# Kernel optimization log

Hardware: AMD Instinct MI355X
Metric: run time of the kernel (lower is better)

Reference implementation:

```python
import jax, jax.numpy as jnp
import numpy as np

TEMPERATURE = 0.1
EPS = 1e-8  # torch CosineSimilarity eps


def setup_inputs() -> dict:
    key = jax.random.key(0)
    y = jax.random.normal(key, (8192, 256), dtype=jnp.float32)
    return {"y": y}


def reference(y):
    # y: (2n, d), rows 2i and 2i+1 are positive pairs
    N = y.shape[0]
    norms = jnp.maximum(jnp.linalg.norm(y, axis=1, keepdims=True), EPS)
    yn = y / norms  # (N, d)
    sim = yn @ yn.T  # (N, N) cosine similarity
    e = jnp.exp(sim / TEMPERATURE)
    # denominator: column-sum excluding diagonal (mask eye==0)
    denom = e.sum(axis=0) - jnp.diagonal(e)  # (N,)
    # positive pair index: row 2i -> 2i+1, row 2i+1 -> 2i (XOR with 1)
    row_idx = jnp.arange(N)
    col_idx = row_idx ^ 1
    pos = e[row_idx, col_idx]  # (N,)
    loss = -jnp.log(pos / denom)
    return loss.mean()
```

## Files before the change

### kernel.cpp

```cpp
#include <hip/hip_runtime.h>
#include <hip/hip_bf16.h>
#include <cstdint>

typedef __attribute__((ext_vector_type(4))) float f32x4;

#define DIM 256
#define TINV 10.0f
#define EXP2C 14.426950408889634f
#define BM 128
#define BN 128
#define BK 64
#define NSLOT 64
#define NRED 128

__global__ void nt_normalize(const float* __restrict__ y, uint8_t* __restrict__ ynq,
                             int N) {
    int tid = threadIdx.x;
    int wave = tid >> 6, lane = tid & 63;
    int row = blockIdx.x * 4 + wave;
    float4 v = ((const float4*)(y + (size_t)row * DIM))[lane];
    float ss = v.x * v.x + v.y * v.y + v.z * v.z + v.w * v.w;
#pragma unroll
    for (int off = 1; off < 64; off <<= 1) ss += __shfl_xor(ss, off);
    float inv = 1.0f / fmaxf(sqrtf(ss), 1e-8f);
    int w = __builtin_amdgcn_cvt_pk_fp8_f32(v.x * inv, v.y * inv, 0, false);
    w = __builtin_amdgcn_cvt_pk_fp8_f32(v.z * inv, v.w * inv, w, true);
    ((int*)(ynq + (size_t)row * DIM))[lane] = w;
}

__launch_bounds__(512, 8)
__global__ void nt_gemm(const uint8_t* __restrict__ ynq, float* __restrict__ P,
                        float* __restrict__ posterm, int N) {
    const int nt = N / BN;
    const int T = nt * (nt + 1) / 2;
    int orig = blockIdx.x;
    int q = T >> 3, r = T & 7;
    int xcd = orig & 7, loc = orig >> 3;
    int t = (xcd < r ? xcd * (q + 1) : r * (q + 1) + (xcd - r) * q) + loc;
    int s = T - 1 - t;
    float f = sqrtf(8.0f * (float)s + 1.0f);
    int j = (int)((f - 1.0f) * 0.5f);
    while ((j + 1) * (j + 2) / 2 <= s) ++j;
    while (j * (j + 1) / 2 > s) --j;
    int k = s - j * (j + 1) / 2;
    int by = nt - 1 - j, bx = nt - 1 - k;

    __shared__ __align__(16) uint8_t As[BM * BK];
    __shared__ __align__(16) uint8_t Bs[BN * BK];
    __shared__ float rowpart[4][BM];
    __shared__ float colpart[2][BN];

    int r0 = by * BM, c0 = bx * BN;
    int tid = threadIdx.x;
    int wave = tid >> 6, lane = tid & 63;
    int wr = wave >> 2, wc = wave & 3;
    int l16 = lane & 15, lg = lane >> 4;

    int srow = tid >> 2, scc = tid & 3;
    int sgc = scc ^ ((srow >> 1) & 3);

    int swz[2];
#pragma unroll
    for (int kk = 0; kk < 2; ++kk)
        swz[kk] = (((kk * 2 + (lg >> 1)) ^ ((l16 >> 1) & 3)) * 16) + (lg & 1) * 8;

    int arow[4], brow[2];
#pragma unroll
    for (int m = 0; m < 4; ++m) arow[m] = (wr * 64 + m * 16 + l16) * BK;
#pragma unroll
    for (int n = 0; n < 2; ++n) brow[n] = (wc * 32 + n * 16 + l16) * BK;

    f32x4 acc[4][2] = {};

    for (int k0 = 0; k0 < DIM; k0 += BK) {
        if (k0) __syncthreads();
        {
            const uint8_t* srcA = ynq + (size_t)(r0 + srow) * DIM + k0 + sgc * 16;
            __builtin_amdgcn_global_load_lds(
                (const __attribute__((address_space(1))) uint32_t*)srcA,
                (__attribute__((address_space(3))) uint32_t*)(As + wave * 1024), 16, 0, 0);
            const uint8_t* srcB = ynq + (size_t)(c0 + srow) * DIM + k0 + sgc * 16;
            __builtin_amdgcn_global_load_lds(
                (const __attribute__((address_space(1))) uint32_t*)srcB,
                (__attribute__((address_space(3))) uint32_t*)(Bs + wave * 1024), 16, 0, 0);
        }
        __syncthreads();

#pragma unroll
        for (int kk = 0; kk < 2; ++kk) {
            long a[4], b[2];
#pragma unroll
            for (int m = 0; m < 4; ++m) a[m] = *(const long*)(As + arow[m] + swz[kk]);
#pragma unroll
            for (int n = 0; n < 2; ++n) b[n] = *(const long*)(Bs + brow[n] + swz[kk]);
#pragma unroll
            for (int m = 0; m < 4; ++m)
#pragma unroll
                for (int n = 0; n < 2; ++n)
                    acc[m][n] = __builtin_amdgcn_mfma_f32_16x16x32_fp8_fp8(
                        a[m], b[n], acc[m][n], 0, 0, 0);
        }
    }

    bool diag = (by == bx);
    float colacc0 = 0.0f, colacc1 = 0.0f;
    float rp[16];
#pragma unroll
    for (int m = 0; m < 4; ++m) {
#pragma unroll
        for (int r2 = 0; r2 < 4; ++r2) {
            int grow = r0 + wr * 64 + m * 16 + lg * 4 + r2;
            float s0, s1;
            {
                float S = acc[m][0][r2];
                float e = __builtin_amdgcn_exp2f(S * EXP2C);
                if (diag) {
                    int gcol = c0 + wc * 32 + l16;
                    if (gcol == grow) e = 0.0f;
                    if (gcol == (grow ^ 1)) posterm[grow] = -S * TINV;
                }
                s0 = e; colacc0 += e;
            }
            {
                float S = acc[m][1][r2];
                float e = __builtin_amdgcn_exp2f(S * EXP2C);
                if (diag) {
                    int gcol = c0 + wc * 32 + 16 + l16;
                    if (gcol == grow) e = 0.0f;
                    if (gcol == (grow ^ 1)) posterm[grow] = -S * TINV;
                }
                s1 = e; colacc1 += e;
            }
            rp[m * 4 + r2] = s0 + s1;
        }
    }
    int b0 = l16 & 1, b1 = (l16 >> 1) & 1, b2 = (l16 >> 2) & 1, b3 = (l16 >> 3) & 1;
    float t8[8];
#pragma unroll
    for (int i = 0; i < 8; ++i) {
        float send = b0 ? rp[2 * i] : rp[2 * i + 1];
        float keep = b0 ? rp[2 * i + 1] : rp[2 * i];
        t8[i] = keep + __shfl_xor(send, 1);
    }
    float t4[4];
#pragma unroll
    for (int i = 0; i < 4; ++i) {
        float send = b1 ? t8[2 * i] : t8[2 * i + 1];
        float keep = b1 ? t8[2 * i + 1] : t8[2 * i];
        t4[i] = keep + __shfl_xor(send, 2);
    }
    float t2[2];
#pragma unroll
    for (int i = 0; i < 2; ++i) {
        float send = b2 ? t4[2 * i] : t4[2 * i + 1];
        float keep = b2 ? t4[2 * i + 1] : t4[2 * i];
        t2[i] = keep + __shfl_xor(send, 4);
    }
    {
        float send = b3 ? t2[0] : t2[1];
        float keep = b3 ? t2[1] : t2[0];
        float rsum = keep + __shfl_xor(send, 8);
        int row_w = ((l16 >> 2) & 3) * 16 + lg * 4 + (l16 & 3);
        rowpart[wc][wr * 64 + row_w] = rsum;
    }
    colacc0 += __shfl_xor(colacc0, 16); colacc0 += __shfl_xor(colacc0, 32);
    colacc1 += __shfl_xor(colacc1, 16); colacc1 += __shfl_xor(colacc1, 32);
    if (!diag && lane < 16) {
        colpart[wr][wc * 32 + lane] = colacc0;
        colpart[wr][wc * 32 + 16 + lane] = colacc1;
    }
    __syncthreads();
    if (tid < BM) {
        P[(size_t)bx * N + r0 + tid] =
            rowpart[0][tid] + rowpart[1][tid] + rowpart[2][tid] + rowpart[3][tid];
    } else if (tid < 2 * BM && !diag) {
        int lcol = tid - BM;
        P[(size_t)by * N + c0 + lcol] = colpart[0][lcol] + colpart[1][lcol];
    }
}

__global__ void nt_reduce_final(const float* __restrict__ P,
                                const float* __restrict__ posterm,
                                float* __restrict__ blockpart,
                                unsigned* __restrict__ cnt,
                                float* __restrict__ out, int N) {
    int lane = threadIdx.x;
    int row = blockIdx.x * 64 + lane;
    float s = 0.0f;
#pragma unroll
    for (int jj = 0; jj < NSLOT; ++jj) s += P[(size_t)jj * N + row];
    float v = posterm[row] + logf(s);
#pragma unroll
    for (int off = 1; off < 64; off <<= 1) v += __shfl_xor(v, off);
    unsigned ticket = 0;
    if (lane == 0) {
        blockpart[blockIdx.x] = v;
        __threadfence();
        ticket = atomicAdd(cnt, 1u);
    }
    ticket = __shfl(ticket, 0);
    if ((ticket & (NRED - 1u)) == NRED - 1u) {
        __threadfence();
        float w = __hip_atomic_load(&blockpart[lane], __ATOMIC_RELAXED,
                                    __HIP_MEMORY_SCOPE_AGENT) +
                  __hip_atomic_load(&blockpart[lane + 64], __ATOMIC_RELAXED,
                                    __HIP_MEMORY_SCOPE_AGENT);
#pragma unroll
        for (int off = 1; off < 64; off <<= 1) w += __shfl_xor(w, off);
        if (lane == 0) out[0] = w / (float)N;
    }
}

extern "C" void kernel_launch(void* const* d_in, const int* in_sizes, int n_in,
                              void* d_out, int out_size, void* d_ws, size_t ws_size,
                              hipStream_t stream) {
    const float* y = (const float*)d_in[0];
    int N = in_sizes[0] / DIM;
    int nt = N / BN;
    uint8_t* ynq = (uint8_t*)d_ws;
    float* posterm = (float*)((char*)d_ws + (size_t)N * DIM);
    float* P = posterm + N;
    float* blockpart = P + (size_t)nt * N;
    unsigned* cnt = (unsigned*)(blockpart + NRED);
    float* out = (float*)d_out;

    nt_normalize<<<N / 4, 256, 0, stream>>>(y, ynq, N);
    int T = nt * (nt + 1) / 2;
    nt_gemm<<<T, 512, 0, stream>>>(ynq, P, posterm, N);
    nt_reduce_final<<<NRED, 64, 0, stream>>>(P, posterm, blockpart, cnt, out, N);
}
```

Baseline: 36.38 us.

## Double-buffer LDS tiles with manual vmcnt waits and MFMA priority boost

Splits the A/B shared-memory tiles into two buffers and unrolls the four K steps by hand. The global-to-LDS load for the next K chunk is issued while the current chunk is being multiplied, with explicit vmcnt waits and raw barriers in place of __syncthreads. s_setprio raises wave priority around the MFMA section. The aim is to hide global load latency behind MFMA work. The cost is twice the LDS per block, which may reduce occupancy, and the hand-written waitcnt ordering relies on the compiler not adding or reordering other memory ops.

```diff
diff --git a/kernel.cpp b/kernel.cpp
--- a/kernel.cpp
+++ b/kernel.cpp
@@ -45,8 +45,8 @@
     int k = s - j * (j + 1) / 2;
     int by = nt - 1 - j, bx = nt - 1 - k;
 
-    __shared__ __align__(16) uint8_t As[BM * BK];
-    __shared__ __align__(16) uint8_t Bs[BN * BK];
+    __shared__ __align__(16) uint8_t As[2][BM * BK];
+    __shared__ __align__(16) uint8_t Bs[2][BN * BK];
     __shared__ float rowpart[4][BM];
     __shared__ float colpart[2][BN];
 
@@ -72,35 +72,64 @@
 
     f32x4 acc[4][2] = {};
 
-    for (int k0 = 0; k0 < DIM; k0 += BK) {
-        if (k0) __syncthreads();
-        {
-            const uint8_t* srcA = ynq + (size_t)(r0 + srow) * DIM + k0 + sgc * 16;
-            __builtin_amdgcn_global_load_lds(
-                (const __attribute__((address_space(1))) uint32_t*)srcA,
-                (__attribute__((address_space(3))) uint32_t*)(As + wave * 1024), 16, 0, 0);
-            const uint8_t* srcB = ynq + (size_t)(c0 + srow) * DIM + k0 + sgc * 16;
-            __builtin_amdgcn_global_load_lds(
-                (const __attribute__((address_space(1))) uint32_t*)srcB,
-                (__attribute__((address_space(3))) uint32_t*)(Bs + wave * 1024), 16, 0, 0);
-        }
-        __syncthreads();
-
-#pragma unroll
-        for (int kk = 0; kk < 2; ++kk) {
-            long a[4], b[2];
-#pragma unroll
-            for (int m = 0; m < 4; ++m) a[m] = *(const long*)(As + arow[m] + swz[kk]);
-#pragma unroll
-            for (int n = 0; n < 2; ++n) b[n] = *(const long*)(Bs + brow[n] + swz[kk]);
-#pragma unroll
-            for (int m = 0; m < 4; ++m)
-#pragma unroll
-                for (int n = 0; n < 2; ++n)
-                    acc[m][n] = __builtin_amdgcn_mfma_f32_16x16x32_fp8_fp8(
-                        a[m], b[n], acc[m][n], 0, 0, 0);
-        }
-    }
+#define STAGE(b, k0)                                                                \
+    {                                                                               \
+        const uint8_t* srcA = ynq + (size_t)(r0 + srow) * DIM + (k0) + sgc * 16;    \
+        __builtin_amdgcn_global_load_lds(                                           \
+            (const __attribute__((address_space(1))) uint32_t*)srcA,                \
+            (__attribute__((address_space(3))) uint32_t*)(As[b] + wave * 1024),     \
+            16, 0, 0);                                                              \
+        const uint8_t* srcB = ynq + (size_t)(c0 + srow) * DIM + (k0) + sgc * 16;    \
+        __builtin_amdgcn_global_load_lds(                                           \
+            (const __attribute__((address_space(1))) uint32_t*)srcB,                \
+            (__attribute__((address_space(3))) uint32_t*)(Bs[b] + wave * 1024),     \
+            16, 0, 0);                                                              \
+    }
+
+#define COMPUTE(b)                                                                  \
+    {                                                                               \
+        __builtin_amdgcn_s_setprio(1);                                              \
+        _Pragma("unroll")                                                           \
+        for (int kk = 0; kk < 2; ++kk) {                                            \
+            long a[4], b2[2];                                                       \
+            _Pragma("unroll")                                                       \
+            for (int m = 0; m < 4; ++m)                                             \
+                a[m] = *(const long*)(As[b] + arow[m] + swz[kk]);                   \
+            _Pragma("unroll")                                                       \
+            for (int n = 0; n < 2; ++n)                                             \
+                b2[n] = *(const long*)(Bs[b] + brow[n] + swz[kk]);                  \
+            _Pragma("unroll")                                                       \
+            for (int m = 0; m < 4; ++m)                                             \
+                _Pragma("unroll")                                                   \
+                for (int n = 0; n < 2; ++n)                                         \
+                    acc[m][n] = __builtin_amdgcn_mfma_f32_16x16x32_fp8_fp8(         \
+                        a[m], b2[n], acc[m][n], 0, 0, 0);                           \
+        }                                                                           \
+        __builtin_amdgcn_s_setprio(0);                                              \
+    }
+
+#define WAITV(n) asm volatile("s_waitcnt vmcnt(" #n ")" ::: "memory")
+#define BAR() __builtin_amdgcn_s_barrier()
+
+    STAGE(0, 0);
+    STAGE(1, 64);
+    WAITV(2); BAR();
+    COMPUTE(0);
+    BAR();
+    STAGE(0, 128);
+    WAITV(2); BAR();
+    COMPUTE(1);
+    BAR();
+    STAGE(1, 192);
+    WAITV(2); BAR();
+    COMPUTE(0);
+    WAITV(0); BAR();
+    COMPUTE(1);
+
+#undef STAGE
+#undef COMPUTE
+#undef WAITV
+#undef BAR
 
     bool diag = (by == bx);
     float colacc0 = 0.0f, colacc1 = 0.0f;
```

Measured after the change: 36.38 us. No clear change (-0.0%).

## Permute fp8 row layout for 128-bit LDS A-fragment loads and vectorize final reduce

Applied to the files above, without the earlier changes.

The normalize kernel now stores each fp8 row in a permuted byte order, so one 16-byte LDS read gives the A operands for both k-substeps. The GEMM swizzle changes to match, cutting the LDS instruction count for A by half. The final reduce kernel reads P and posterm as float4 with 32 blocks instead of 128 scalar-reading blocks. This couples the global layout to the MFMA operand order, and correctness depends on the permutation applying identically to A and B so the dot products still match.

```diff
diff --git a/kernel.cpp b/kernel.cpp
--- a/kernel.cpp
+++ b/kernel.cpp
@@ -3,6 +3,7 @@
 #include <cstdint>
 
 typedef __attribute__((ext_vector_type(4))) float f32x4;
+typedef __attribute__((ext_vector_type(2))) long long2_t;
 
 #define DIM 256
 #define TINV 10.0f
@@ -11,7 +12,7 @@
 #define BN 128
 #define BK 64
 #define NSLOT 64
-#define NRED 128
+#define NRED 32
 
 __global__ void nt_normalize(const float* __restrict__ y, uint8_t* __restrict__ ynq,
                              int N) {
@@ -25,7 +26,10 @@
     float inv = 1.0f / fmaxf(sqrtf(ss), 1e-8f);
     int w = __builtin_amdgcn_cvt_pk_fp8_f32(v.x * inv, v.y * inv, 0, false);
     w = __builtin_amdgcn_cvt_pk_fp8_f32(v.z * inv, v.w * inv, w, true);
-    ((int*)(ynq + (size_t)row * DIM))[lane] = w;
+    int u_row = lane >> 1;
+    int addr = (u_row >> 3) * 64 + (((u_row & 7) & 3) << 4) + (((u_row & 7) >> 2) << 3)
+               + ((lane & 1) << 2);
+    *(int*)(ynq + (size_t)row * DIM + addr) = w;
 }
 
 __launch_bounds__(512, 8)
@@ -57,12 +61,9 @@
     int l16 = lane & 15, lg = lane >> 4;
 
     int srow = tid >> 2, scc = tid & 3;
-    int sgc = scc ^ ((srow >> 1) & 3);
-
-    int swz[2];
-#pragma unroll
-    for (int kk = 0; kk < 2; ++kk)
-        swz[kk] = (((kk * 2 + (lg >> 1)) ^ ((l16 >> 1) & 3)) * 16) + (lg & 1) * 8;
+    int sgc = scc ^ (srow & 3);
+
+    int slot16 = (lg ^ (l16 & 3)) * 16;
 
     int arow[4], brow[2];
 #pragma unroll
@@ -86,19 +87,24 @@
         }
         __syncthreads();
 
+        long2_t a2[4];
+#pragma unroll
+        for (int m = 0; m < 4; ++m)
+            a2[m] = *(const long2_t*)(As + arow[m] + slot16);
 #pragma unroll
         for (int kk = 0; kk < 2; ++kk) {
-            long a[4], b[2];
-#pragma unroll
-            for (int m = 0; m < 4; ++m) a[m] = *(const long*)(As + arow[m] + swz[kk]);
-#pragma unroll
-            for (int n = 0; n < 2; ++n) b[n] = *(const long*)(Bs + brow[n] + swz[kk]);
-#pragma unroll
-            for (int m = 0; m < 4; ++m)
+            long b2[2];
+#pragma unroll
+            for (int n = 0; n < 2; ++n)
+                b2[n] = *(const long*)(Bs + brow[n] + slot16 + kk * 8);
+#pragma unroll
+            for (int m = 0; m < 4; ++m) {
+                long am = kk ? a2[m].y : a2[m].x;
 #pragma unroll
                 for (int n = 0; n < 2; ++n)
                     acc[m][n] = __builtin_amdgcn_mfma_f32_16x16x32_fp8_fp8(
-                        a[m], b[n], acc[m][n], 0, 0, 0);
+                        am, b2[n], acc[m][n], 0, 0, 0);
+            }
         }
     }
 
@@ -134,7 +140,7 @@
             rp[m * 4 + r2] = s0 + s1;
         }
     }
-    int b0 = l16 & 1, b1 = (l16 >> 1) & 1, b2 = (l16 >> 2) & 1, b3 = (l16 >> 3) & 1;
+    int b0 = l16 & 1, b1 = (l16 >> 1) & 1, b2_ = (l16 >> 2) & 1, b3 = (l16 >> 3) & 1;
     float t8[8];
 #pragma unroll
     for (int i = 0; i < 8; ++i) {
@@ -152,8 +158,8 @@
     float t2[2];
 #pragma unroll
     for (int i = 0; i < 2; ++i) {
-        float send = b2 ? t4[2 * i] : t4[2 * i + 1];
-        float keep = b2 ? t4[2 * i + 1] : t4[2 * i];
+        float send = b2_ ? t4[2 * i] : t4[2 * i + 1];
+        float keep = b2_ ? t4[2 * i + 1] : t4[2 * i];
         t2[i] = keep + __shfl_xor(send, 4);
     }
     {
@@ -185,11 +191,14 @@
                                 unsigned* __restrict__ cnt,
                                 float* __restrict__ out, int N) {
     int lane = threadIdx.x;
-    int row = blockIdx.x * 64 + lane;
-    float s = 0.0f;
-#pragma unroll
-    for (int jj = 0; jj < NSLOT; ++jj) s += P[(size_t)jj * N + row];
-    float v = posterm[row] + logf(s);
+    int gid = blockIdx.x * 64 + lane;
+    f32x4 ps = {0.0f, 0.0f, 0.0f, 0.0f};
+#pragma unroll
+    for (int jj = 0; jj < NSLOT; ++jj)
+        ps += ((const f32x4*)(P + (size_t)jj * N))[gid];
+    f32x4 pt = ((const f32x4*)posterm)[gid];
+    float v = (pt[0] + logf(ps[0])) + (pt[1] + logf(ps[1])) +
+              (pt[2] + logf(ps[2])) + (pt[3] + logf(ps[3]));
 #pragma unroll
     for (int off = 1; off < 64; off <<= 1) v += __shfl_xor(v, off);
     unsigned ticket = 0;
@@ -201,10 +210,10 @@
     ticket = __shfl(ticket, 0);
     if ((ticket & (NRED - 1u)) == NRED - 1u) {
         __threadfence();
-        float w = __hip_atomic_load(&blockpart[lane], __ATOMIC_RELAXED,
-                                    __HIP_MEMORY_SCOPE_AGENT) +
-                  __hip_atomic_load(&blockpart[lane + 64], __ATOMIC_RELAXED,
-                                    __HIP_MEMORY_SCOPE_AGENT);
+        float w = (lane < NRED)
+                      ? __hip_atomic_load(&blockpart[lane], __ATOMIC_RELAXED,
+                                          __HIP_MEMORY_SCOPE_AGENT)
+                      : 0.0f;
 #pragma unroll
         for (int off = 1; off < 64; off <<= 1) w += __shfl_xor(w, off);
         if (lane == 0) out[0] = w / (float)N;
```

Result: faster. 34.30 us (-5.7%).
